# Performance work log

Hardware: AMD Instinct MI355X
Metric: run time of the kernel (lower is better)

## Reference

```python
import jax, jax.numpy as jnp
import numpy as np

NEG_SLOPE = 0.2  # PyG GATConv default leaky_relu slope


def gat_conv(x, edge_index, W, a_src, a_dst, b):
    """PyG GATConv (heads=1, concat=True, add_self_loops=True, dropout=0)."""
    N = x.shape[0]
    loops = jnp.arange(N, dtype=edge_index.dtype)
    src = jnp.concatenate([edge_index[0], loops])  # [Ef]
    dst = jnp.concatenate([edge_index[1], loops])  # [Ef]
    h = x @ W  # [N, Dout]
    alpha_src = h @ a_src  # [N]
    alpha_dst = h @ a_dst  # [N]
    logits = jax.nn.leaky_relu(alpha_src[src] + alpha_dst[dst], NEG_SLOPE)  # [Ef]
    # segment softmax over edges grouped by destination node
    m = jax.ops.segment_max(logits, dst, num_segments=N)
    e = jnp.exp(logits - m[dst])
    denom = jax.ops.segment_sum(e, dst, num_segments=N)  # >0: every node has a self-loop
    alpha = e / denom[dst]  # [Ef]
    out = jax.ops.segment_sum(alpha[:, None] * h[src], dst, num_segments=N)
    return out + b


def global_mean_pool(x, batch, num_graphs):
    s = jax.ops.segment_sum(x, batch, num_segments=num_graphs)
    cnt = jax.ops.segment_sum(jnp.ones((x.shape[0],), x.dtype), batch, num_segments=num_graphs)
    return s / jnp.maximum(cnt, 1.0)[:, None]


NUM_GRAPHS = 64


def setup_inputs() -> dict:
    key = jax.random.key(0)
    ks = jax.random.split(key, 12)
    N, E, D = 50000, 600000, 128
    x = jax.random.normal(ks[0], (N, D), dtype=jnp.float32)
    edge_index = jax.random.randint(ks[1], (2, E), 0, N, dtype=jnp.int32)
    edge_weight = jax.random.uniform(ks[2], (E,), dtype=jnp.float32)
    batch = jnp.sort(jax.random.randint(ks[3], (N,), 0, NUM_GRAPHS, dtype=jnp.int32))
    sc = 1.0 / np.sqrt(D)
    W0 = jax.random.normal(ks[4], (D, D), dtype=jnp.float32) * sc
    a_src0 = jax.random.normal(ks[5], (D,), dtype=jnp.float32) * sc
    a_dst0 = jax.random.normal(ks[6], (D,), dtype=jnp.float32) * sc
    b0 = jnp.zeros((D,), dtype=jnp.float32)
    W1 = jax.random.normal(ks[7], (D, D), dtype=jnp.float32) * sc
    a_src1 = jax.random.normal(ks[8], (D,), dtype=jnp.float32) * sc
    a_dst1 = jax.random.normal(ks[9], (D,), dtype=jnp.float32) * sc
    b1 = jnp.zeros((D,), dtype=jnp.float32)
    return {"x": x, "edge_index": edge_index, "edge_weight": edge_weight, "batch": batch,
            "W0": W0, "a_src0": a_src0, "a_dst0": a_dst0, "b0": b0,
            "W1": W1, "a_src1": a_src1, "a_dst1": a_dst1, "b1": b1}


def reference(x, edge_index, edge_weight, batch, W0, a_src0, a_dst0, b0, W1, a_src1, a_dst1, b1):
    # layer 0 (relu_layers_index=[0] -> ReLU after layer 0)
    out = gat_conv(x, edge_index, W0, a_src0, a_dst0, b0)
    out = jax.nn.relu(out)
    emb0 = global_mean_pool(out, batch, NUM_GRAPHS)
    # layer 1 (no relu, no dropout)
    out = gat_conv(out, edge_index, W1, a_src1, a_dst1, b1)
    emb1 = global_mean_pool(out, batch, NUM_GRAPHS)
    return (emb0, emb1)
```

## Files before the change

kernel.cpp:

```cpp
#include <hip/hip_runtime.h>

typedef unsigned int u32;
typedef unsigned short u16;

typedef short bf16x8 __attribute__((ext_vector_type(8)));
typedef float f32x4 __attribute__((ext_vector_type(4)));
typedef float f32x2 __attribute__((ext_vector_type(2)));

__device__ __forceinline__ float bl(u32 u){ return __uint_as_float(u << 16); }
__device__ __forceinline__ float bh(u32 u){ return __uint_as_float(u & 0xffff0000u); }
__device__ __forceinline__ float b16f(u16 r){ return __uint_as_float(((u32)r) << 16); }
__device__ __forceinline__ u16 f2b(float f){
  u32 u = __float_as_uint(f);
  u32 r = (u + 0x7fffu + ((u >> 16) & 1u)) >> 16;
  return (u16)r;
}
__device__ __forceinline__ u32 pk2(float a, float b){
  return (u32)f2b(a) | ((u32)f2b(b) << 16);
}
__device__ __forceinline__ void fma8(float* acc, float e2, uint2 h){
  f32x2 p0 = __builtin_amdgcn_cvt_pk_f32_fp8((int)h.x, 0);
  f32x2 p1 = __builtin_amdgcn_cvt_pk_f32_fp8((int)h.x, 1);
  f32x2 p2 = __builtin_amdgcn_cvt_pk_f32_fp8((int)h.y, 0);
  f32x2 p3 = __builtin_amdgcn_cvt_pk_f32_fp8((int)h.y, 1);
  acc[0]=fmaf(e2,p0.x,acc[0]); acc[1]=fmaf(e2,p0.y,acc[1]);
  acc[2]=fmaf(e2,p1.x,acc[2]); acc[3]=fmaf(e2,p1.y,acc[3]);
  acc[4]=fmaf(e2,p2.x,acc[4]); acc[5]=fmaf(e2,p2.y,acc[5]);
  acc[6]=fmaf(e2,p3.x,acc[6]); acc[7]=fmaf(e2,p3.y,acc[7]);
}

#define NEG_SLOPE 0.2f
#define CAP 64


__global__ __launch_bounds__(256) void scatdet_k(const int* __restrict__ ei,
    int* __restrict__ deg, int* __restrict__ csrc, int E,
    const u32* __restrict__ x, int* __restrict__ flag)
{
  if (blockIdx.x == 0){
    __shared__ int cnt;
    if (threadIdx.x == 0) cnt = 0;
    __syncthreads();
    u32 w = x[threadIdx.x];
    int e = (int)((w >> 7) & 0xFFu);
    if (e >= 110 && e <= 135) atomicAdd(&cnt, 1);
    __syncthreads();
    if (threadIdx.x == 0) *flag = (cnt >= 128) ? 1 : 0;
  }
  int t = blockIdx.x*256 + threadIdx.x;
  if (t >= E) return;
  int d = ei[E + t];
  int pos = atomicAdd(deg + d, 1);
  if (pos < CAP) csrc[d*CAP + pos] = ei[t];
}

template<bool XEXT, bool KPERM>
__global__ __launch_bounds__(256) void gemm_k(const void* __restrict__ Xv,
    const void* __restrict__ Wv, const void* __restrict__ av, const void* __restrict__ dv,
    const int* __restrict__ flag,
    u32* __restrict__ Hb, float* __restrict__ As, float* __restrict__ Ad, int N)
{
  __shared__ u16 Wt[128*136];
  const int tid = threadIdx.x;
  const int isbf = *flag;

  if (isbf){
    const u32* Wp = (const u32*)Wv;
    #pragma unroll
    for (int i = 0; i < 16; i++){
      int idx = tid + i*256;
      u32 p = Wp[idx];
      int k = idx >> 6, n2 = idx & 63;
      int pos = KPERM ? ((k & 15)*8 + (k >> 4)) : k;
      Wt[(2*n2)*136 + pos]   = (u16)(p & 0xffffu);
      Wt[(2*n2+1)*136 + pos] = (u16)(p >> 16);
    }
  } else {
    const float* Wf = (const float*)Wv;
    #pragma unroll
    for (int i = 0; i < 64; i++){
      int idx = tid + i*256;
      int k = idx >> 7, n = idx & 127;
      int pos = KPERM ? ((k & 15)*8 + (k >> 4)) : k;
      Wt[n*136 + pos] = f2b(Wf[idx]);
    }
  }
  __syncthreads();

  const int wv = tid >> 6, L = tid & 63;
  const int row0 = (blockIdx.x*4 + wv) * 16;
  if (row0 >= N) return;
  const int nl = L & 15, quad = L >> 4;

  bf16x8 af[4];
  if (!XEXT || isbf){
    const uint4* Xr = (const uint4*)(((const u32*)Xv) + (long)row0*64);
    #pragma unroll
    for (int kb = 0; kb < 4; kb++)
      af[kb] = *(const bf16x8*)&Xr[nl*16 + kb*4 + quad];
  } else {
    const float* Xf = ((const float*)Xv) + (long)(row0 + nl)*128;
    #pragma unroll
    for (int kb = 0; kb < 4; kb++){
      const float4* p = (const float4*)(Xf + kb*32 + quad*8);
      float4 f0 = p[0], f1 = p[1];
      uint4 tmp = make_uint4(pk2(f0.x,f0.y), pk2(f0.z,f0.w), pk2(f1.x,f1.y), pk2(f1.z,f1.w));
      af[kb] = *(const bf16x8*)&tmp;
    }
  }

  f32x4 acc[8];
  #pragma unroll
  for (int nt = 0; nt < 8; nt++) acc[nt] = (f32x4){0.f,0.f,0.f,0.f};
  #pragma unroll
  for (int nt = 0; nt < 8; nt++){
    #pragma unroll
    for (int kb = 0; kb < 4; kb++){
      bf16x8 bf = *(const bf16x8*)&Wt[(nt*16 + nl)*136 + kb*32 + quad*8];
      acc[nt] = __builtin_amdgcn_mfma_f32_16x16x32_bf16(af[kb], bf, acc[nt], 0, 0, 0);
    }
  }

  float ps[4] = {0.f,0.f,0.f,0.f}, pd[4] = {0.f,0.f,0.f,0.f};
  #pragma unroll
  for (int nt = 0; nt < 8; nt++){
    int col = nt*16 + nl;
    float a_ = isbf ? b16f(((const u16*)av)[col]) : ((const float*)av)[col];
    float d_ = isbf ? b16f(((const u16*)dv)[col]) : ((const float*)dv)[col];
    #pragma unroll
    for (int r = 0; r < 4; r++){
      ps[r] = fmaf(acc[nt][r], a_, ps[r]);
      pd[r] = fmaf(acc[nt][r], d_, pd[r]);
    }
  }
  #pragma unroll
  for (int off = 1; off < 16; off <<= 1){
    #pragma unroll
    for (int r = 0; r < 4; r++){
      ps[r] += __shfl_xor(ps[r], off);
      pd[r] += __shfl_xor(pd[r], off);
    }
  }
  if (nl == 0){
    #pragma unroll
    for (int r = 0; r < 4; r++){
      As[row0 + quad*4 + r] = ps[r];
      Ad[row0 + quad*4 + r] = pd[r];
    }
  }

  #pragma unroll
  for (int r = 0; r < 4; r++){
    long row = row0 + quad*4 + r;
    int w0 = 0, w1 = 0;
    w0 = __builtin_amdgcn_cvt_pk_fp8_f32(acc[0][r], acc[1][r], w0, 0);
    w0 = __builtin_amdgcn_cvt_pk_fp8_f32(acc[2][r], acc[3][r], w0, 1);
    w1 = __builtin_amdgcn_cvt_pk_fp8_f32(acc[4][r], acc[5][r], w1, 0);
    w1 = __builtin_amdgcn_cvt_pk_fp8_f32(acc[6][r], acc[7][r], w1, 1);
    uint2 v = make_uint2((u32)w0, (u32)w1);
    *(uint2*)(Hb + row*32 + nl*2) = v;
  }
}

template<bool RELU>
__global__ __launch_bounds__(256) void gath_k(const int* __restrict__ deg,
    const int* __restrict__ csrc, const float* __restrict__ As, const float* __restrict__ Ad,
    const u32* __restrict__ Hb, const void* __restrict__ bv, const int* __restrict__ flag,
    u32* __restrict__ Ob, int N)
{
  long t = (long)blockIdx.x*256 + threadIdx.x;
  int node = (int)(t >> 4), q = (int)(t & 15);
  if (node >= N) return;
  const int base = threadIdx.x & 48;
  const float ad = Ad[node];
  float l = As[node] + ad;
  l = l > 0.f ? l : NEG_SLOPE * l;
  float e = __expf(l);
  float acc[8];
  {
    uint2 hv = ((const uint2*)(Hb + (long)node*32))[q];
    f32x2 p0 = __builtin_amdgcn_cvt_pk_f32_fp8((int)hv.x, 0);
    f32x2 p1 = __builtin_amdgcn_cvt_pk_f32_fp8((int)hv.x, 1);
    f32x2 p2 = __builtin_amdgcn_cvt_pk_f32_fp8((int)hv.y, 0);
    f32x2 p3 = __builtin_amdgcn_cvt_pk_f32_fp8((int)hv.y, 1);
    acc[0]=e*p0.x; acc[1]=e*p0.y; acc[2]=e*p1.x; acc[3]=e*p1.y;
    acc[4]=e*p2.x; acc[5]=e*p2.y; acc[6]=e*p3.x; acc[7]=e*p3.y;
  }
  float den = e;
  int dg = deg[node]; if (dg > CAP) dg = CAP;
  const int* row = csrc + (long)node*CAP;
  for (int jb = 0; jb < dg; jb += 16){
    int m = dg - jb; if (m > 16) m = 16;
    int sj = node; float evq = 0.f;
    if (q < m){
      sj = row[jb + q];
      float l2 = As[sj] + ad;
      l2 = l2 > 0.f ? l2 : NEG_SLOPE * l2;
      evq = __expf(l2);
    }
    for (int i = 0; i < m; i += 4){
      float e0 = __shfl(evq, base + i);
      float e1 = __shfl(evq, base + i + 1);
      float e2 = __shfl(evq, base + i + 2);
      float e3 = __shfl(evq, base + i + 3);
      int   s0 = __shfl(sj,  base + i);
      int   s1 = __shfl(sj,  base + i + 1);
      int   s2 = __shfl(sj,  base + i + 2);
      int   s3 = __shfl(sj,  base + i + 3);
      uint2 h0 = ((const uint2*)(Hb + (long)s0*32))[q];
      uint2 h1 = ((const uint2*)(Hb + (long)s1*32))[q];
      uint2 h2 = ((const uint2*)(Hb + (long)s2*32))[q];
      uint2 h3 = ((const uint2*)(Hb + (long)s3*32))[q];
      den += (e0 + e1) + (e2 + e3);
      fma8(acc, e0, h0);
      fma8(acc, e1, h1);
      fma8(acc, e2, h2);
      fma8(acc, e3, h3);
    }
  }
  float inv = 1.f / den;
  float b[8];
  if (*flag){
    const u16* bp = (const u16*)bv;
    #pragma unroll
    for (int i = 0; i < 8; i++) b[i] = b16f(bp[i*16 + q]);
  } else {
    const float* bp = (const float*)bv;
    #pragma unroll
    for (int i = 0; i < 8; i++) b[i] = bp[i*16 + q];
  }
  float o[8];
  #pragma unroll
  for (int i = 0; i < 8; i++){
    o[i] = fmaf(acc[i], inv, b[i]);
    if (RELU) o[i] = fmaxf(o[i], 0.f);
  }
  uint4 w = make_uint4(pk2(o[0],o[1]), pk2(o[2],o[3]), pk2(o[4],o[5]), pk2(o[6],o[7]));
  *(uint4*)&Ob[(long)node*64 + q*4] = w;
}

__global__ __launch_bounds__(256) void pool2_k(const u32* __restrict__ Ob,
    const int* __restrict__ batch, float* __restrict__ psum, int N)
{
  const int tid = threadIdx.x;
  const int wv = tid >> 6, lane = tid & 63;
  const int start = blockIdx.x * 128;
  const int end = min(start + 128, N);
  float2 acc = make_float2(0.f, 0.f);
  int cur = -1;
  for (int node = start + wv; node < end; node += 4){
    int gid = batch[node];
    if (gid != cur){
      if (cur >= 0){
        atomicAdd(&psum[cur*128 + lane*2],     acc.x);
        atomicAdd(&psum[cur*128 + lane*2 + 1], acc.y);
      }
      cur = gid; acc = make_float2(0.f, 0.f);
    }
    u32 p = Ob[(long)node*64 + lane];
    acc.x += bl(p); acc.y += bh(p);
  }
  if (cur >= 0){
    atomicAdd(&psum[cur*128 + lane*2],     acc.x);
    atomicAdd(&psum[cur*128 + lane*2 + 1], acc.y);
  }
}

__global__ __launch_bounds__(256) void fin_k(const float* __restrict__ ps0,
    const float* __restrict__ ps1, const int* __restrict__ batch, int N,
    const int* __restrict__ flag, void* __restrict__ out)
{
  int t = blockIdx.x*256 + threadIdx.x;
  if (t >= 8192) return;
  int g = t >> 7, pos = t & 127;
  int c = ((pos & 7) << 4) + (pos >> 3);
  int lo = 0, hi = N;
  while (lo < hi){ int mid = (lo + hi) >> 1; if (batch[mid] < g) lo = mid + 1; else hi = mid; }
  int a = lo;
  lo = 0; hi = N;
  while (lo < hi){ int mid = (lo + hi) >> 1; if (batch[mid] < g + 1) lo = mid + 1; else hi = mid; }
  int cc = lo - a;
  float cf = (float)(cc < 1 ? 1 : cc);
  float v0 = ps0[t] / cf, v1 = ps1[t] / cf;
  if (*flag){
    u16* o = (u16*)out;
    o[g*128 + c] = f2b(v0); o[8192 + g*128 + c] = f2b(v1);
  } else {
    float* o = (float*)out;
    o[g*128 + c] = v0; o[8192 + g*128 + c] = v1;
  }
}

extern "C" void kernel_launch(void* const* d_in, const int* in_sizes, int n_in,
                              void* d_out, int out_size, void* d_ws, size_t ws_size,
                              hipStream_t stream)
{
  const void* x    = d_in[0];
  const int* ei    = (const int*)d_in[1];
  const int* batch = (const int*)d_in[3];
  const void* W0  = d_in[4];
  const void* as0 = d_in[5];
  const void* ad0 = d_in[6];
  const void* b0  = d_in[7];
  const void* W1  = d_in[8];
  const void* as1 = d_in[9];
  const void* ad1 = d_in[10];
  const void* b1  = d_in[11];

  const int N  = in_sizes[0] / 128;
  const int E  = in_sizes[1] / 2;

  char* ws = (char*)d_ws;
  size_t off = 0;
  auto al = [&](size_t bytes){ size_t o = off; off += (bytes + 255) & ~(size_t)255; return o; };
  u32*   Hb    = (u32*)(ws + al((size_t)N*32*4));
  u32*   Ob    = (u32*)(ws + al((size_t)N*64*4));
  float* As    = (float*)(ws + al((size_t)N*4));
  float* Ad    = (float*)(ws + al((size_t)N*4));
  int*   csrc  = (int*)(ws + al((size_t)N*CAP*4));
  char*  z0    = ws + al((size_t)N*4 + 2*64*128*4);
  int*   deg   = (int*)z0;
  float* ps0   = (float*)(z0 + (size_t)N*4);
  float* ps1   = ps0 + 8192;
  int*   flag  = (int*)(ws + al(256));
  if (off > ws_size) return;

  hipMemsetAsync(deg, 0, (size_t)N*4 + 2*64*128*4, stream);

  const int gB   = (N/16 + 3) / 4;
  const int eB   = (E + 255) / 256;
  const int nvB16= (N*16 + 255) / 256;
  const int pB   = (N + 127) / 128;

  scatdet_k<<<eB, 256, 0, stream>>>(ei, deg, csrc, E, (const u32*)x, flag);

  gemm_k<true, false><<<gB, 256, 0, stream>>>(x, W0, as0, ad0, flag, Hb, As, Ad, N);
  gath_k<true><<<nvB16, 256, 0, stream>>>(deg, csrc, As, Ad, Hb, b0, flag, Ob, N);
  pool2_k<<<pB, 256, 0, stream>>>(Ob, batch, ps0, N);

  gemm_k<false, true><<<gB, 256, 0, stream>>>(Ob, W1, as1, ad1, flag, Hb, As, Ad, N);
  gath_k<false><<<nvB16, 256, 0, stream>>>(deg, csrc, As, Ad, Hb, b1, flag, Ob, N);
  pool2_k<<<pB, 256, 0, stream>>>(Ob, batch, ps1, N);

  fin_k<<<32, 256, 0, stream>>>(ps0, ps1, batch, N, flag, d_out);
}
```

Baseline: 221.3 us.

## Merge independent kernels by splitting grid blocks between scatter/gemm0 and pool/gemm1

The edge-scatter kernel and the first GEMM become one launch whose blocks branch by index range. The layer-0 pooling and the second GEMM are merged the same way, and each GEMM block now detects the input dtype itself. This removes two launches and lets independent work share the GPU at the same time. The merged kernels carry the GEMM's large shared-memory allocation for every block, so the scatter and pool blocks may get lower occupancy.

```diff
diff --git a/kernel.cpp b/kernel.cpp
--- a/kernel.cpp
+++ b/kernel.cpp
@@ -33,36 +33,25 @@
 #define CAP 64
 
 
-__global__ __launch_bounds__(256) void scatdet_k(const int* __restrict__ ei,
-    int* __restrict__ deg, int* __restrict__ csrc, int E,
-    const u32* __restrict__ x, int* __restrict__ flag)
-{
-  if (blockIdx.x == 0){
-    __shared__ int cnt;
-    if (threadIdx.x == 0) cnt = 0;
-    __syncthreads();
-    u32 w = x[threadIdx.x];
-    int e = (int)((w >> 7) & 0xFFu);
-    if (e >= 110 && e <= 135) atomicAdd(&cnt, 1);
-    __syncthreads();
-    if (threadIdx.x == 0) *flag = (cnt >= 128) ? 1 : 0;
-  }
-  int t = blockIdx.x*256 + threadIdx.x;
-  if (t >= E) return;
-  int d = ei[E + t];
-  int pos = atomicAdd(deg + d, 1);
-  if (pos < CAP) csrc[d*CAP + pos] = ei[t];
+__device__ __forceinline__ int block_detect(const u32* __restrict__ x){
+  __shared__ int cnt_;
+  if (threadIdx.x == 0) cnt_ = 0;
+  __syncthreads();
+  u32 w = x[threadIdx.x];
+  int e = (int)((w >> 7) & 0xFFu);
+  if (e >= 110 && e <= 135) atomicAdd(&cnt_, 1);
+  __syncthreads();
+  return (cnt_ >= 128) ? 1 : 0;
 }
 
 template<bool XEXT, bool KPERM>
-__global__ __launch_bounds__(256) void gemm_k(const void* __restrict__ Xv,
-    const void* __restrict__ Wv, const void* __restrict__ av, const void* __restrict__ dv,
-    const int* __restrict__ flag,
+__device__ __forceinline__ void gemm_body(int gb, int isbf,
+    const void* __restrict__ Xv, const void* __restrict__ Wv,
+    const void* __restrict__ av, const void* __restrict__ dv,
     u32* __restrict__ Hb, float* __restrict__ As, float* __restrict__ Ad, int N)
 {
   __shared__ u16 Wt[128*136];
   const int tid = threadIdx.x;
-  const int isbf = *flag;
 
   if (isbf){
     const u32* Wp = (const u32*)Wv;
@@ -88,7 +77,7 @@
   __syncthreads();
 
   const int wv = tid >> 6, L = tid & 63;
-  const int row0 = (blockIdx.x*4 + wv) * 16;
+  const int row0 = (gb*4 + wv) * 16;
   if (row0 >= N) return;
   const int nl = L & 15, quad = L >> 4;
 
@@ -160,6 +149,68 @@
     uint2 v = make_uint2((u32)w0, (u32)w1);
     *(uint2*)(Hb + row*32 + nl*2) = v;
   }
+}
+
+__device__ __forceinline__ void pool_body(const u32* __restrict__ Ob,
+    const int* __restrict__ batch, float* __restrict__ psum, int N)
+{
+  const int tid = threadIdx.x;
+  const int wv = tid >> 6, lane = tid & 63;
+  const int start = blockIdx.x * 128;
+  const int end = min(start + 128, N);
+  float2 acc = make_float2(0.f, 0.f);
+  int cur = -1;
+  for (int node = start + wv; node < end; node += 4){
+    int gid = batch[node];
+    if (gid != cur){
+      if (cur >= 0){
+        atomicAdd(&psum[cur*128 + lane*2],     acc.x);
+        atomicAdd(&psum[cur*128 + lane*2 + 1], acc.y);
+      }
+      cur = gid; acc = make_float2(0.f, 0.f);
+    }
+    u32 p = Ob[(long)node*64 + lane];
+    acc.x += bl(p); acc.y += bh(p);
+  }
+  if (cur >= 0){
+    atomicAdd(&psum[cur*128 + lane*2],     acc.x);
+    atomicAdd(&psum[cur*128 + lane*2 + 1], acc.y);
+  }
+}
+
+__global__ __launch_bounds__(256) void scatgemm0_k(
+    const int* __restrict__ ei, int* __restrict__ deg, int* __restrict__ csrc, int E, int eB,
+    const u32* __restrict__ x, int* __restrict__ flag,
+    const void* __restrict__ W0, const void* __restrict__ as0, const void* __restrict__ ad0,
+    u32* __restrict__ Hb, float* __restrict__ As, float* __restrict__ Ad, int N)
+{
+  if ((int)blockIdx.x < eB){
+    int t = blockIdx.x*256 + threadIdx.x;
+    if (t < E){
+      int d = ei[E + t];
+      int pos = atomicAdd(deg + d, 1);
+      if (pos < CAP) csrc[d*CAP + pos] = ei[t];
+    }
+    return;
+  }
+  const int gb = blockIdx.x - eB;
+  int isbf = block_detect(x);
+  if (gb == 0 && threadIdx.x == 0) *flag = isbf;
+  gemm_body<true, false>(gb, isbf, x, W0, as0, ad0, Hb, As, Ad, N);
+}
+
+__global__ __launch_bounds__(256) void poolgemm1_k(
+    const u32* __restrict__ Ob, const int* __restrict__ batch, float* __restrict__ ps0, int pB,
+    const void* __restrict__ W1, const void* __restrict__ as1, const void* __restrict__ ad1,
+    const int* __restrict__ flag,
+    u32* __restrict__ Hb, float* __restrict__ As, float* __restrict__ Ad, int N)
+{
+  if ((int)blockIdx.x < pB){
+    pool_body(Ob, batch, ps0, N);
+    return;
+  }
+  const int gb = blockIdx.x - pB;
+  gemm_body<false, true>(gb, *flag, Ob, W1, as1, ad1, Hb, As, Ad, N);
 }
 
 template<bool RELU>
@@ -242,28 +293,7 @@
 __global__ __launch_bounds__(256) void pool2_k(const u32* __restrict__ Ob,
     const int* __restrict__ batch, float* __restrict__ psum, int N)
 {
-  const int tid = threadIdx.x;
-  const int wv = tid >> 6, lane = tid & 63;
-  const int start = blockIdx.x * 128;
-  const int end = min(start + 128, N);
-  float2 acc = make_float2(0.f, 0.f);
-  int cur = -1;
-  for (int node = start + wv; node < end; node += 4){
-    int gid = batch[node];
-    if (gid != cur){
-      if (cur >= 0){
-        atomicAdd(&psum[cur*128 + lane*2],     acc.x);
-        atomicAdd(&psum[cur*128 + lane*2 + 1], acc.y);
-      }
-      cur = gid; acc = make_float2(0.f, 0.f);
-    }
-    u32 p = Ob[(long)node*64 + lane];
-    acc.x += bl(p); acc.y += bh(p);
-  }
-  if (cur >= 0){
-    atomicAdd(&psum[cur*128 + lane*2],     acc.x);
-    atomicAdd(&psum[cur*128 + lane*2 + 1], acc.y);
-  }
+  pool_body(Ob, batch, psum, N);
 }
 
 __global__ __launch_bounds__(256) void fin_k(const float* __restrict__ ps0,
@@ -332,13 +362,12 @@
   const int nvB16= (N*16 + 255) / 256;
   const int pB   = (N + 127) / 128;
 
-  scatdet_k<<<eB, 256, 0, stream>>>(ei, deg, csrc, E, (const u32*)x, flag);
-
-  gemm_k<true, false><<<gB, 256, 0, stream>>>(x, W0, as0, ad0, flag, Hb, As, Ad, N);
+  scatgemm0_k<<<eB + gB, 256, 0, stream>>>(ei, deg, csrc, E, eB,
+      (const u32*)x, flag, W0, as0, ad0, Hb, As, Ad, N);
   gath_k<true><<<nvB16, 256, 0, stream>>>(deg, csrc, As, Ad, Hb, b0, flag, Ob, N);
-  pool2_k<<<pB, 256, 0, stream>>>(Ob, batch, ps0, N);
-
-  gemm_k<false, true><<<gB, 256, 0, stream>>>(Ob, W1, as1, ad1, flag, Hb, As, Ad, N);
+
+  poolgemm1_k<<<pB + gB, 256, 0, stream>>>(Ob, batch, ps0, pB,
+      W1, as1, ad1, flag, Hb, As, Ad, N);
   gath_k<false><<<nvB16, 256, 0, stream>>>(deg, csrc, As, Ad, Hb, b1, flag, Ob, N);
   pool2_k<<<pB, 256, 0, stream>>>(Ob, batch, ps1, N);
 
```

Result: faster. 208.8 us (-5.7%).
